# Optimization experiments

Measured on AMD Instinct MI355X. Metric: run time of the kernel, lower is better.

Reference implementation:

```python
import jax, jax.numpy as jnp
import numpy as np

HIDDEN = 256
TOTAL_NUM = 32
VOCAB = TOTAL_NUM + 3  # BOS, EOS, PAD appended
IDX_PAD = TOTAL_NUM + 2
BETA = 1.0


def setup_inputs() -> dict:
    key = jax.random.key(0)
    k1, k2, k3, k4, k5 = jax.random.split(key, 5)
    B, P, T = 16, 8, 256
    event_obs = jax.random.randint(k1, (B, P, T), 0, VOCAB)
    dtime_obs = jax.random.uniform(k2, (B, P, T), dtype=jnp.float32)
    scale = 1.0 / np.sqrt(HIDDEN)
    Emb = jax.random.normal(k3, (VOCAB, HIDDEN), dtype=jnp.float32) * scale
    # CTLSTMCell: Linear(2H -> 7H) producing i, f, o, z, i_bar, f_bar, decay
    W = jax.random.normal(k4, (7 * HIDDEN, 2 * HIDDEN), dtype=jnp.float32) * scale
    b = jax.random.normal(k5, (7 * HIDDEN,), dtype=jnp.float32) * 0.01
    return {"event_obs": event_obs, "dtime_obs": dtime_obs, "Emb": Emb, "W": W, "b": b}


def _ct_lstm_right2left(event_obs, dtime_obs, Emb, W, b):
    B, P, T = event_obs.shape
    H = Emb.shape[1]
    dt = Emb.dtype
    emb_all = Emb[event_obs]  # [B,P,T,H]
    # steps process i = T-1 ... 1 (reverse); xs are time-major for i in [1, T-1]
    xs = (
        jnp.moveaxis(emb_all[:, :, 1:], 2, 0),      # [T-1,B,P,H]
        jnp.moveaxis(dtime_obs[:, :, 1:], 2, 0),    # [T-1,B,P]
        jnp.moveaxis(event_obs[:, :, 1:], 2, 0),    # [T-1,B,P]
    )
    init = (jnp.zeros((B, P, H), dt), jnp.zeros((B, P, H), dt), jnp.zeros((B, P, H), dt))

    def step(carry, x):
        c_plus, cbar_next, h_plus = carry
        emb_i, dtime_i, ev_i = x
        z = jnp.concatenate([emb_i, h_plus], axis=-1) @ W.T + b  # [B,P,7H]
        gi, gf, go, gz, gib, gfb, gd = jnp.split(z, 7, axis=-1)
        gi = jax.nn.sigmoid(gi)
        gf = jax.nn.sigmoid(gf)
        go = jax.nn.sigmoid(go)
        gz = jnp.tanh(gz)
        gib = jax.nn.sigmoid(gib)
        gfb = jax.nn.sigmoid(gfb)
        gd = jax.nn.softplus(BETA * gd) / BETA  # decay rate > 0
        cell_i = gf * c_plus + gi * gz
        cbar_i = gfb * cbar_next + gib * gz
        h_minus = go * jnp.tanh(cell_i)                       # decay(dt=0)
        decay = jnp.exp(-gd * dtime_i[..., None])
        c_im1 = cbar_i + (cell_i - cbar_i) * decay            # decay(dt=dtime_i)
        h_im1 = go * jnp.tanh(c_im1)
        mask = (ev_i != IDX_PAD).astype(dt)[..., None]
        c_im1 = c_im1 * mask
        cbar_i = cbar_i * mask
        h_im1 = h_im1 * mask
        ys = (cell_i, cbar_i, gd, go, h_im1, h_minus)
        return (c_im1, cbar_i, h_im1), ys

    _, ys = jax.lax.scan(step, init, xs, reverse=True)
    # ys[k] corresponds to i = k+1, matching torch's reversed append order
    return tuple(jnp.moveaxis(y, 0, 2) for y in ys)  # each [B,P,T-1,H]


def reference(event_obs, dtime_obs, Emb, W, b):
    all_cell, all_cell_bar, all_gate_decay, all_gate_output, all_hidden, all_hidden_after_update = \
        _ct_lstm_right2left(event_obs, dtime_obs, Emb, W, b)
    return (all_cell, all_cell_bar, all_gate_decay, all_gate_output, all_hidden, all_hidden_after_update)
```

## Files before the change

### kernel.cpp

```cpp
#include <hip/hip_runtime.h>
#include <cstddef>
#include <cstdint>


typedef _Float16 hf;
typedef _Float16 f16x8 __attribute__((ext_vector_type(8)));
typedef float    f32x4 __attribute__((ext_vector_type(4)));

#define HID  256
#define R7   1792
#define TT   256
#define NPAD 34
#define HBUF_HF 4096

__device__ __forceinline__ float sigf(float x) { return 1.0f / (1.0f + __expf(-x)); }
__device__ __forceinline__ float tanh_f(float x) { return 1.0f - 2.0f / (__expf(2.0f * x) + 1.0f); }
__device__ __forceinline__ float softplusf(float x) {
  return fmaxf(x, 0.0f) + __logf(1.0f + __expf(-fabsf(x)));
}

__global__ __launch_bounds__(256) void repack_mfma(const float* __restrict__ W,
                                                   f16x8* __restrict__ Wf) {
  int idx  = blockIdx.x * 256 + threadIdx.x;
  int lane = idx & 63;
  int kt   = (idx >> 6) & 7;
  int gb   = idx >> 9;
  int g    = gb % 7;
  int b    = gb / 7;
  int row  = g * HID + b * 16 + (lane & 15);
  int k0   = kt * 32 + (lane >> 4) * 8;
  const float* src = W + (size_t)row * 512 + 256 + k0;
  f16x8 o;
#pragma unroll
  for (int e = 0; e < 8; ++e) o[e] = (hf)src[e];
  Wf[idx] = o;
}

__global__ __launch_bounds__(256) void ew_kernel(const float* __restrict__ Emb,
                                                 const float* __restrict__ W,
                                                 const float* __restrict__ bias,
                                                 float* __restrict__ EW) {
  int wid  = (blockIdx.x * 256 + threadIdx.x) >> 6;
  int lane = threadIdx.x & 63;
  int o    = wid * 4;
#pragma unroll
  for (int qq = 0; qq < 4; ++qq, ++o) {
    int e = o / R7;
    int r = o - e * R7;
    const float4 ev4 = *(const float4*)(Emb + e * HID + lane * 4);
    const float4 wv4 = *(const float4*)(W + (size_t)r * 512 + lane * 4);
    float acc = ev4.x * wv4.x + ev4.y * wv4.y + ev4.z * wv4.z + ev4.w * wv4.w;
#pragma unroll
    for (int m = 32; m >= 1; m >>= 1) acc += __shfl_xor(acc, m, 64);
    if (lane == 0) EW[o] = acc + bias[r];
  }
}

__global__ __launch_bounds__(256, 1) void scan_mfma(
    const int* __restrict__ event, const float* __restrict__ dtime,
    const float* __restrict__ EW, const f16x8* __restrict__ Wf,
    hf* __restrict__ hbuf, int* __restrict__ flags,
    float* __restrict__ out) {
  const int tid = threadIdx.x;
  const int b   = blockIdx.x & 15;
  const int p   = blockIdx.x >> 4;
  const int j0  = b * 16;
  const int wid = tid >> 6, lane = tid & 63;
  const int seq = tid >> 4, jj = tid & 15;
  const int j   = j0 + jj;
  const int q   = lane >> 4, nn = lane & 15;

  __shared__ int   evs[32][TT];
  __shared__ float dts[32][TT];
  __shared__ __align__(16) float gbuf[7][16][20];

#pragma unroll 4
  for (int r = 0; r < 32; ++r) {
    evs[r][tid] = event[(size_t)(p * 32 + r) * TT + tid];
    dts[r][tid] = dtime[(size_t)(p * 32 + r) * TT + tid];
  }

  const int  g0  = 2 * wid;
  const bool two = (wid < 3);
  f16x8 B0[8], B1[8];
  {
    const f16x8* wsrc = Wf + (size_t)((b * 7 + g0) * 8) * 64 + lane;
#pragma unroll
    for (int kt = 0; kt < 8; ++kt) B0[kt] = wsrc[kt * 64];
    if (two) {
#pragma unroll
      for (int kt = 0; kt < 8; ++kt) B1[kt] = wsrc[(8 + kt) * 64];
    }
  }
  __syncthreads();

  int* flb = flags + p * 64;
  hf*  hpb = hbuf + (size_t)p * 4 * HBUF_HF;

  const int off16 = ((j >> 5) * 64 + seq + 16 * ((j >> 3) & 3)) * 8 + (j & 7);
  const size_t OS = 8355840;

  float cp0 = 0.f, cb0 = 0.f, cp1 = 0.f, cb1 = 0.f;
  int pr = 0;

  auto body = [&](const int c, const int it, float& cp, float& cb) {
    const int   i  = 255 - it, t = i - 1;
    const int   cs = c * 16 + seq;
    const int   ev = evs[cs][i];
    const float dt = dts[cs][i];
    int* flc = flb + c * 32;

    asm volatile("s_waitcnt vmcnt(0)" ::: "memory");
    __builtin_amdgcn_sched_barrier(0);
    if (it > 0) {
      int pv = (nn == b) ? 0x7fffffff : pr;
      if (!__all(pv >= it)) {
        int gd = 0;
        for (;;) {
          int v = (nn == b) ? 0x7fffffff
                : __hip_atomic_load(&flc[nn], __ATOMIC_RELAXED,
                                    __HIP_MEMORY_SCOPE_AGENT);
          if (__all(v >= it) || ++gd > (1 << 20)) break;
        }
      }
    }

    f16x8 av[8];
    if (it > 0) {
      const hf* hp = hpb + (size_t)(c * 2 + (it & 1)) * HBUF_HF + (size_t)lane * 8;
#pragma unroll
      for (int kt = 0; kt < 8; ++kt)
        asm volatile("global_load_dwordx4 %0, %1, off sc0 sc1"
                     : "=v"(av[kt]) : "v"(hp + (size_t)kt * 512));
    }
    float e0[4], e1[4];
#pragma unroll
    for (int r = 0; r < 4; ++r) {
      const int evr = evs[c * 16 + 4 * q + r][i];
      const float* Ep = EW + (size_t)evr * R7 + j0 + nn;
      e0[r] = Ep[g0 * HID];
      e1[r] = two ? Ep[(g0 + 1) * HID] : 0.0f;
    }

    asm volatile("" ::: "memory");
    __builtin_amdgcn_s_barrier();
    asm volatile("" ::: "memory");

    asm volatile("s_waitcnt vmcnt(0)" ::: "memory");
    __builtin_amdgcn_sched_barrier(0);

    if (tid == 0 && (c == 1 || it > 0)) {
      const int fv = (c == 0) ? it : it + 1;
      __hip_atomic_store(&flb[(c ^ 1) * 32 + b], fv, __ATOMIC_RELAXED,
                         __HIP_MEMORY_SCOPE_AGENT);
    }

    f32x4 acc0 = {e0[0], e0[1], e0[2], e0[3]};
    f32x4 acc1 = {e1[0], e1[1], e1[2], e1[3]};
    if (it > 0) {
#pragma unroll
      for (int kt = 0; kt < 8; ++kt) {
        acc0 = __builtin_amdgcn_mfma_f32_16x16x32_f16(av[kt], B0[kt], acc0, 0, 0, 0);
        if (two)
          acc1 = __builtin_amdgcn_mfma_f32_16x16x32_f16(av[kt], B1[kt], acc1, 0, 0, 0);
      }
    }

    *(f32x4*)&gbuf[g0][nn][4 * q] = acc0;
    if (two) *(f32x4*)&gbuf[g0 + 1][nn][4 * q] = acc1;
    asm volatile("s_waitcnt lgkmcnt(0)" ::: "memory");
    __builtin_amdgcn_s_barrier();
    __builtin_amdgcn_sched_barrier(0);

    float zz[7];
#pragma unroll
    for (int g = 0; g < 7; ++g) zz[g] = gbuf[g][jj][seq];
    float gi = sigf(zz[0]), gf = sigf(zz[1]), go = sigf(zz[2]);
    float gz = tanh_f(zz[3]);
    float gib = sigf(zz[4]), gfb = sigf(zz[5]);
    float gd = softplusf(zz[6]);
    float cell = gf * cp + gi * gz;
    float cbar = gfb * cb + gib * gz;
    float hm   = go * tanh_f(cell);
    float dec  = __expf(-gd * dt);
    float cim  = cbar + (cell - cbar) * dec;
    float him  = go * tanh_f(cim);
    float msk  = (ev != NPAD) ? 1.0f : 0.0f;
    float cbm  = cbar * msk;
    float hn   = him * msk;
    cp = cim * msk;
    cb = cbm;

    unsigned short hb16 = __builtin_bit_cast(unsigned short, (hf)hn);
    unsigned nb = __shfl_down((unsigned)hb16, 1, 64);
    if (it < 254 && !(jj & 1)) {
      unsigned pack = (unsigned)hb16 | (nb << 16);
      hf* hw = hpb + (size_t)(c * 2 + ((it + 1) & 1)) * HBUF_HF;
      __hip_atomic_store((unsigned*)(hw + off16), pack, __ATOMIC_RELAXED,
                         __HIP_MEMORY_SCOPE_AGENT);
    }

    pr = __hip_atomic_load(&flb[(c ^ 1) * 32 + nn], __ATOMIC_RELAXED,
                           __HIP_MEMORY_SCOPE_AGENT);

    float* o = out + (size_t)(p * 32 + cs) * 65280 + (size_t)t * HID + j;
    o[0] = cell; o[OS] = cbm; o[2 * OS] = gd; o[3 * OS] = go;
    o[4 * OS] = hn; o[5 * OS] = hm;
  };

#pragma unroll 1
  for (int it = 0; it < 255; ++it) {
    body(0, it, cp0, cb0);
    body(1, it, cp1, cb1);
  }
}

extern "C" void kernel_launch(void* const* d_in, const int* in_sizes, int n_in,
                              void* d_out, int out_size, void* d_ws, size_t ws_size,
                              hipStream_t stream) {
  const int*   event = (const int*)d_in[0];
  const float* dtime = (const float*)d_in[1];
  const float* Emb   = (const float*)d_in[2];
  const float* W     = (const float*)d_in[3];
  const float* bias  = (const float*)d_in[4];
  float*       out   = (float*)d_out;

  char*  ws = (char*)d_ws;
  f16x8* Wf = (f16x8*)ws;
  float* EW = (float*)(ws + 917504);
  hf*    hb = (hf*)(ws + 917504 + 250880);
  int*   fl = (int*)(ws + 917504 + 250880 + 131072);

  hipMemsetAsync(ws + 917504 + 250880, 0, 131072 + 1024, stream);
  repack_mfma<<<224, 256, 0, stream>>>(W, Wf);
  ew_kernel<<<3920, 256, 0, stream>>>(Emb, W, bias, EW);
  scan_mfma<<<64, 256, 0, stream>>>(event, dtime, EW, Wf, hb, fl, out);
}
```

Baseline: 1.146 ms.

## Prefetch next sequence-group h and EW inputs during gate math

Restructures the recurrent scan so the flag wait and the h-buffer and EW loads for the next interleaved sequence group are issued right after the MFMA step. Those loads then overlap with the current group's elementwise gate math instead of sitting at the head of each step. The flag read becomes an asm load issued earlier, the h stores become explicit sc0/sc1 stores, and the output stores become nontemporal. This carries a risk of subtle ordering bugs around the partial vmcnt waits and the cross-block flag protocol.

Result: slower. 1.369 ms (+19.5%).

```diff
diff --git a/kernel.cpp b/kernel.cpp
--- a/kernel.cpp
+++ b/kernel.cpp
@@ -101,59 +101,43 @@
   const size_t OS = 8355840;
 
   float cp0 = 0.f, cb0 = 0.f, cp1 = 0.f, cb1 = 0.f;
-  int pr = 0;
-
-  auto body = [&](const int c, const int it, float& cp, float& cb) {
-    const int   i  = 255 - it, t = i - 1;
-    const int   cs = c * 16 + seq;
-    const int   ev = evs[cs][i];
-    const float dt = dts[cs][i];
-    int* flc = flb + c * 32;
-
-    asm volatile("s_waitcnt vmcnt(0)" ::: "memory");
-    __builtin_amdgcn_sched_barrier(0);
-    if (it > 0) {
-      int pv = (nn == b) ? 0x7fffffff : pr;
-      if (!__all(pv >= it)) {
-        int gd = 0;
-        for (;;) {
-          int v = (nn == b) ? 0x7fffffff
-                : __hip_atomic_load(&flc[nn], __ATOMIC_RELAXED,
-                                    __HIP_MEMORY_SCOPE_AGENT);
-          if (__all(v >= it) || ++gd > (1 << 20)) break;
-        }
-      }
-    }
-
-    f16x8 av[8];
-    if (it > 0) {
-      const hf* hp = hpb + (size_t)(c * 2 + (it & 1)) * HBUF_HF + (size_t)lane * 8;
-#pragma unroll
-      for (int kt = 0; kt < 8; ++kt)
-        asm volatile("global_load_dwordx4 %0, %1, off sc0 sc1"
-                     : "=v"(av[kt]) : "v"(hp + (size_t)kt * 512));
-    }
-    float e0[4], e1[4];
+
+  f16x8 av[8];
+#pragma unroll
+  for (int kt = 0; kt < 8; ++kt) av[kt] = (f16x8)(hf)0.0f;
+  float e0[4], e1[4];
+  {
 #pragma unroll
     for (int r = 0; r < 4; ++r) {
-      const int evr = evs[c * 16 + 4 * q + r][i];
+      const int evr = evs[4 * q + r][255];
       const float* Ep = EW + (size_t)evr * R7 + j0 + nn;
       e0[r] = Ep[g0 * HID];
       e1[r] = two ? Ep[(g0 + 1) * HID] : 0.0f;
     }
-
-    asm volatile("" ::: "memory");
+  }
+
+  auto body = [&](const int c, const int it, float& cp, float& cb) {
+    const int   i   = 255 - it, t = i - 1;
+    const int   cs  = c * 16 + seq;
+    const int   ev  = evs[cs][i];
+    const float dt  = dts[cs][i];
+    const int   nc  = c ^ 1;
+    const int   itn = (c == 0) ? it : it + 1;
+    const int   fv  = itn;
+    int* flq = flb + nc * 32;
+    const bool doH = !(c == 0 && it == 0) && !(c == 1 && it == 254);
+    const bool doE = !(c == 1 && it == 254);
+
+    asm volatile("s_waitcnt vmcnt(6)" ::: "memory");
+    __builtin_amdgcn_sched_barrier(0);
     __builtin_amdgcn_s_barrier();
-    asm volatile("" ::: "memory");
-
-    asm volatile("s_waitcnt vmcnt(0)" ::: "memory");
-    __builtin_amdgcn_sched_barrier(0);
-
-    if (tid == 0 && (c == 1 || it > 0)) {
-      const int fv = (c == 0) ? it : it + 1;
-      __hip_atomic_store(&flb[(c ^ 1) * 32 + b], fv, __ATOMIC_RELAXED,
+
+    if (tid == 0 && fv > 0)
+      __hip_atomic_store(&flq[b], fv, __ATOMIC_RELAXED,
                          __HIP_MEMORY_SCOPE_AGENT);
-    }
+    int pr;
+    asm volatile("global_load_dword %0, %1, off sc0 sc1"
+                 : "=v"(pr) : "v"(flq + nn) : "memory");
 
     f32x4 acc0 = {e0[0], e0[1], e0[2], e0[3]};
     f32x4 acc1 = {e1[0], e1[1], e1[2], e1[3]};
@@ -171,6 +155,42 @@
     asm volatile("s_waitcnt lgkmcnt(0)" ::: "memory");
     __builtin_amdgcn_s_barrier();
     __builtin_amdgcn_sched_barrier(0);
+
+    asm volatile("s_waitcnt vmcnt(0)" ::: "memory");
+    __builtin_amdgcn_sched_barrier(0);
+    if (doH && fv > 0) {
+      int pv = (nn == b) ? 0x7fffffff : pr;
+      if (!__all(pv >= fv)) {
+        int gd = 0;
+        for (;;) {
+          int v = (nn == b) ? 0x7fffffff
+                : __hip_atomic_load(&flq[nn], __ATOMIC_RELAXED,
+                                    __HIP_MEMORY_SCOPE_AGENT);
+          if (__all(v >= fv) || ++gd > (1 << 20)) break;
+        }
+      }
+    }
+
+    if (doH) {
+      const hf* hp = hpb + (size_t)(nc * 2 + (itn & 1)) * HBUF_HF + (size_t)lane * 8;
+#pragma unroll
+      for (int kt = 0; kt < 8; ++kt)
+        asm volatile("global_load_dwordx4 %0, %1, off sc0 sc1"
+                     : "=v"(av[kt]) : "v"(hp + (size_t)kt * 512) : "memory");
+    }
+    if (doE) {
+      const int inext = 255 - itn;
+#pragma unroll
+      for (int r = 0; r < 4; ++r) {
+        const int evr = evs[nc * 16 + 4 * q + r][inext];
+        const float* Ep = EW + (size_t)evr * R7 + j0 + nn;
+        asm volatile("global_load_dword %0, %1, off"
+                     : "=v"(e0[r]) : "v"(Ep + g0 * HID) : "memory");
+        if (two)
+          asm volatile("global_load_dword %0, %1, off"
+                       : "=v"(e1[r]) : "v"(Ep + (g0 + 1) * HID) : "memory");
+      }
+    }
 
     float zz[7];
 #pragma unroll
@@ -196,16 +216,17 @@
     if (it < 254 && !(jj & 1)) {
       unsigned pack = (unsigned)hb16 | (nb << 16);
       hf* hw = hpb + (size_t)(c * 2 + ((it + 1) & 1)) * HBUF_HF;
-      __hip_atomic_store((unsigned*)(hw + off16), pack, __ATOMIC_RELAXED,
-                         __HIP_MEMORY_SCOPE_AGENT);
-    }
-
-    pr = __hip_atomic_load(&flb[(c ^ 1) * 32 + nn], __ATOMIC_RELAXED,
-                           __HIP_MEMORY_SCOPE_AGENT);
+      asm volatile("global_store_dword %0, %1, off sc0 sc1"
+                   :: "v"((unsigned*)(hw + off16)), "v"(pack) : "memory");
+    }
 
     float* o = out + (size_t)(p * 32 + cs) * 65280 + (size_t)t * HID + j;
-    o[0] = cell; o[OS] = cbm; o[2 * OS] = gd; o[3 * OS] = go;
-    o[4 * OS] = hn; o[5 * OS] = hm;
+    __builtin_nontemporal_store(cell, o);
+    __builtin_nontemporal_store(cbm, o + OS);
+    __builtin_nontemporal_store(gd, o + 2 * OS);
+    __builtin_nontemporal_store(go, o + 3 * OS);
+    __builtin_nontemporal_store(hn, o + 4 * OS);
+    __builtin_nontemporal_store(hm, o + 5 * OS);
   };
 
 #pragma unroll 1
```

## Cache EW in LDS and relax vmcnt waits to overlap output stores

Applied to the files above, without the earlier changes.

Preloads the per-block slice of the embedding-projection table EW into shared memory, so each step reads gate biases from LDS instead of global memory. Replaces the full vmcnt(0) wait at the top of each step with vmcnt(6), letting the six output stores stay in flight while the flag load completes. The block barrier and flag publication now sit at the start of the step. Stores and the flag load are issued as inline asm with explicit cache bits. The counted wait depends on exact instruction ordering, which makes the inter-block handshake more fragile.

After: 1.002 ms. -12.6%, faster.

```diff
diff --git a/kernel.cpp b/kernel.cpp
--- a/kernel.cpp
+++ b/kernel.cpp
@@ -73,11 +73,17 @@
   __shared__ int   evs[32][TT];
   __shared__ float dts[32][TT];
   __shared__ __align__(16) float gbuf[7][16][20];
+  __shared__ float ews[35 * 7 * 17];
 
 #pragma unroll 4
   for (int r = 0; r < 32; ++r) {
     evs[r][tid] = event[(size_t)(p * 32 + r) * TT + tid];
     dts[r][tid] = dtime[(size_t)(p * 32 + r) * TT + tid];
+  }
+  for (int idx = tid; idx < 35 * 112; idx += 256) {
+    int e  = idx / 112, r = idx - e * 112;
+    int g  = r >> 4, n2 = r & 15;
+    ews[(e * 7 + g) * 17 + n2] = EW[(size_t)e * R7 + g * HID + j0 + n2];
   }
 
   const int  g0  = 2 * wid;
@@ -92,6 +98,13 @@
       for (int kt = 0; kt < 8; ++kt) B1[kt] = wsrc[(8 + kt) * 64];
     }
   }
+  asm volatile("s_waitcnt vmcnt(0)" ::: "memory");
+  __builtin_amdgcn_sched_barrier(0);
+#pragma unroll
+  for (int kt = 0; kt < 8; ++kt) {
+    asm volatile("" :: "v"(B0[kt]));
+    if (two) asm volatile("" :: "v"(B1[kt]));
+  }
   __syncthreads();
 
   int* flb = flags + p * 64;
@@ -104,21 +117,28 @@
   int pr = 0;
 
   auto body = [&](const int c, const int it, float& cp, float& cb) {
-    const int   i  = 255 - it, t = i - 1;
-    const int   cs = c * 16 + seq;
-    const int   ev = evs[cs][i];
-    const float dt = dts[cs][i];
-    int* flc = flb + c * 32;
-
-    asm volatile("s_waitcnt vmcnt(0)" ::: "memory");
+    const int   i   = 255 - it, t = i - 1;
+    const int   cs  = c * 16 + seq;
+    const int   ev  = evs[cs][i];
+    const float dt  = dts[cs][i];
+    const int   nc  = c ^ 1;
+    const int   itn = (c == 0) ? it : it + 1;
+
+    asm volatile("s_waitcnt vmcnt(6)" : "+v"(pr) :: "memory");
     __builtin_amdgcn_sched_barrier(0);
+    __builtin_amdgcn_s_barrier();
+
+    if (tid == 0 && itn > 0)
+      __hip_atomic_store(&flb[nc * 32 + b], itn, __ATOMIC_RELAXED,
+                         __HIP_MEMORY_SCOPE_AGENT);
+
     if (it > 0) {
       int pv = (nn == b) ? 0x7fffffff : pr;
       if (!__all(pv >= it)) {
         int gd = 0;
         for (;;) {
           int v = (nn == b) ? 0x7fffffff
-                : __hip_atomic_load(&flc[nn], __ATOMIC_RELAXED,
+                : __hip_atomic_load(&flb[c * 32 + nn], __ATOMIC_RELAXED,
                                     __HIP_MEMORY_SCOPE_AGENT);
           if (__all(v >= it) || ++gd > (1 << 20)) break;
         }
@@ -131,28 +151,23 @@
 #pragma unroll
       for (int kt = 0; kt < 8; ++kt)
         asm volatile("global_load_dwordx4 %0, %1, off sc0 sc1"
-                     : "=v"(av[kt]) : "v"(hp + (size_t)kt * 512));
-    }
+                     : "=v"(av[kt]) : "v"(hp + (size_t)kt * 512) : "memory");
+    }
+
     float e0[4], e1[4];
 #pragma unroll
     for (int r = 0; r < 4; ++r) {
-      const int evr = evs[c * 16 + 4 * q + r][i];
-      const float* Ep = EW + (size_t)evr * R7 + j0 + nn;
-      e0[r] = Ep[g0 * HID];
-      e1[r] = two ? Ep[(g0 + 1) * HID] : 0.0f;
-    }
-
-    asm volatile("" ::: "memory");
-    __builtin_amdgcn_s_barrier();
-    asm volatile("" ::: "memory");
+      const int evr  = evs[c * 16 + 4 * q + r][i];
+      const int base = (evr * 7 + g0) * 17 + nn;
+      e0[r] = ews[base];
+      e1[r] = two ? ews[base + 17] : 0.0f;
+    }
 
     asm volatile("s_waitcnt vmcnt(0)" ::: "memory");
     __builtin_amdgcn_sched_barrier(0);
-
-    if (tid == 0 && (c == 1 || it > 0)) {
-      const int fv = (c == 0) ? it : it + 1;
-      __hip_atomic_store(&flb[(c ^ 1) * 32 + b], fv, __ATOMIC_RELAXED,
-                         __HIP_MEMORY_SCOPE_AGENT);
+    if (it > 0) {
+#pragma unroll
+      for (int kt = 0; kt < 8; ++kt) asm volatile("" : "+v"(av[kt]));
     }
 
     f32x4 acc0 = {e0[0], e0[1], e0[2], e0[3]};
@@ -196,16 +211,20 @@
     if (it < 254 && !(jj & 1)) {
       unsigned pack = (unsigned)hb16 | (nb << 16);
       hf* hw = hpb + (size_t)(c * 2 + ((it + 1) & 1)) * HBUF_HF;
-      __hip_atomic_store((unsigned*)(hw + off16), pack, __ATOMIC_RELAXED,
-                         __HIP_MEMORY_SCOPE_AGENT);
-    }
-
-    pr = __hip_atomic_load(&flb[(c ^ 1) * 32 + nn], __ATOMIC_RELAXED,
-                           __HIP_MEMORY_SCOPE_AGENT);
+      asm volatile("global_store_dword %0, %1, off sc0 sc1"
+                   :: "v"((unsigned*)(hw + off16)), "v"(pack) : "memory");
+    }
+
+    asm volatile("global_load_dword %0, %1, off sc0 sc1"
+                 : "=v"(pr) : "v"(flb + nc * 32 + nn) : "memory");
 
     float* o = out + (size_t)(p * 32 + cs) * 65280 + (size_t)t * HID + j;
-    o[0] = cell; o[OS] = cbm; o[2 * OS] = gd; o[3 * OS] = go;
-    o[4 * OS] = hn; o[5 * OS] = hm;
+    asm volatile("global_store_dword %0, %1, off" :: "v"(o), "v"(cell) : "memory");
+    asm volatile("global_store_dword %0, %1, off" :: "v"(o + OS), "v"(cbm) : "memory");
+    asm volatile("global_store_dword %0, %1, off" :: "v"(o + 2 * OS), "v"(gd) : "memory");
+    asm volatile("global_store_dword %0, %1, off" :: "v"(o + 3 * OS), "v"(go) : "memory");
+    asm volatile("global_store_dword %0, %1, off" :: "v"(o + 4 * OS), "v"(hn) : "memory");
+    asm volatile("global_store_dword %0, %1, off" :: "v"(o + 5 * OS), "v"(hm) : "memory");
   };
 
 #pragma unroll 1
```
